# Optimization experiments

Measured on AMD Instinct MI355X. Metric: run time of the kernel, lower is better.

Reference implementation:

```python
import jax, jax.numpy as jnp
import numpy as np

B, C, W = 8, 128, 4096
REDUCTION = 8
D = C // REDUCTION  # 16


def setup_inputs() -> dict:
    key = jax.random.key(0)
    ks = jax.random.split(key, 7)
    scale = 0.05
    return {
        "x": jax.random.normal(ks[0], (B, C, W), dtype=jnp.float32),
        "Wq": jax.random.normal(ks[1], (D, C), dtype=jnp.float32) * scale,
        "bq": jax.random.normal(ks[2], (D,), dtype=jnp.float32) * scale,
        "Wk": jax.random.normal(ks[3], (D, C), dtype=jnp.float32) * scale,
        "bk": jax.random.normal(ks[4], (D,), dtype=jnp.float32) * scale,
        "Wv": jax.random.normal(ks[5], (C, C), dtype=jnp.float32) * scale,
        "bv": jax.random.normal(ks[6], (C,), dtype=jnp.float32) * scale,
    }


def reference(x, Wq, bq, Wk, bk, Wv, bv):
    # 1x1 Conv1d == per-position linear over channel axis
    q = jnp.einsum('dc,bcw->bdw', Wq, x) + bq[None, :, None]   # [B, D, W]
    k = jnp.einsum('dc,bcw->bdw', Wk, x) + bk[None, :, None]   # [B, D, W]
    v = jnp.einsum('oc,bcw->bow', Wv, x) + bv[None, :, None]   # [B, C, W]
    scale = D ** (-0.5)
    # scores[b,i,j] = q[b,:,i] . k[b,:,j]
    scores = jnp.einsum('bdi,bdj->bij', q, k) * scale          # [B, W, W]
    attn = jax.nn.softmax(scores, axis=-1)
    # torch.bmm(value, attn): context[b,c,w] = sum_j v[b,c,j] * attn[b,j,w]
    context = jnp.einsum('bcj,bjw->bcw', v, attn)              # [B, C, W]
    return context + x
```

## Files before the change

### kernel.cpp

```cpp
#include <hip/hip_runtime.h>

#define B_ 8
#define C_ 128
#define W_ 4096
#define D_ 16
#define SCALE2 0.3606737602222409f

typedef short bf16x8 __attribute__((ext_vector_type(8)));
typedef float f32x4 __attribute__((ext_vector_type(4)));

__device__ __forceinline__ unsigned short f2bf(float f) {
    unsigned int u = __float_as_uint(f);
    u += 0x7fffu + ((u >> 16) & 1u);
    return (unsigned short)(u >> 16);
}
__device__ __forceinline__ unsigned int pk2bf(float lo, float hi) {
    return __builtin_amdgcn_perm(__float_as_uint(hi), __float_as_uint(lo), 0x07060302u);
}
__device__ __forceinline__ bf16x8 u4_to_bf8(unsigned int a, unsigned int b,
                                            unsigned int c, unsigned int d) {
    union { uint4 u; bf16x8 v; } t;
    t.u = make_uint4(a, b, c, d);
    return t.v;
}
__device__ __forceinline__ bf16x8 exp2pack(f32x4 a, f32x4 b) {
    return u4_to_bf8(
        pk2bf(__builtin_amdgcn_exp2f(a[0]), __builtin_amdgcn_exp2f(a[1])),
        pk2bf(__builtin_amdgcn_exp2f(a[2]), __builtin_amdgcn_exp2f(a[3])),
        pk2bf(__builtin_amdgcn_exp2f(b[0]), __builtin_amdgcn_exp2f(b[1])),
        pk2bf(__builtin_amdgcn_exp2f(b[2]), __builtin_amdgcn_exp2f(b[3])));
}
__device__ __forceinline__ int xswz(int j, int c8) {
    return c8 ^ (j & 7) ^ ((j >> 3) & 7);
}

__global__ __launch_bounds__(256) void prep(
    const float* __restrict__ Wq, const float* __restrict__ Wk, const float* __restrict__ Wv,
    unsigned short* __restrict__ Wvbf, unsigned short* __restrict__ Wqkbf)
{
    int g = blockIdx.x * 256 + threadIdx.x;
    const float* src; unsigned short* dst; float sc = 1.0f;
    if (g < 4096)      { src = Wv + g * 4;            dst = Wvbf + g * 4; }
    else if (g < 4608) { int t = g - 4096; src = Wq + t * 4; dst = Wqkbf + t * 4; sc = SCALE2; }
    else               { int t = g - 4608; src = Wk + t * 4; dst = Wqkbf + 2048 + t * 4; }
    float4 v = *(const float4*)src;
    unsigned short h[4] = {f2bf(v.x * sc), f2bf(v.y * sc), f2bf(v.z * sc), f2bf(v.w * sc)};
    *(ushort4*)dst = *(ushort4*)h;
}

__global__ __launch_bounds__(256) void proj(
    const float* __restrict__ x, const unsigned short* __restrict__ Wvbf,
    const unsigned short* __restrict__ Wqkbf,
    const float* __restrict__ bqp, const float* __restrict__ bkp, const float* __restrict__ bvp,
    unsigned short* __restrict__ qws, unsigned short* __restrict__ kws,
    unsigned short* __restrict__ vws)
{
    __shared__ unsigned short xbf[64 * 128];
    __shared__ unsigned short outs[128 * 72];

    int b  = blockIdx.x & 7;
    int j0 = (blockIdx.x >> 3) * 64;
    int tid = threadIdx.x;
    int wid = tid >> 6, lane = tid & 63, n = lane & 15, q4 = lane >> 4;

#pragma unroll
    for (int i = 0; i < 8; i++) {
        int c = (tid >> 4) + 16 * i;
        int jc = (tid & 15) * 4;
        float4 t = *(const float4*)(x + (size_t)(b * C_ + c) * W_ + j0 + jc);
        float tv[4] = {t.x, t.y, t.z, t.w};
#pragma unroll
        for (int cc = 0; cc < 4; cc++) {
            int j = jc + cc;
            xbf[j * 128 + xswz(j, c >> 3) * 8 + (c & 7)] = f2bf(tv[cc]);
        }
    }
    __syncthreads();

    const f32x4 zero = {0.f, 0.f, 0.f, 0.f};
    f32x4 accv[2][4]; f32x4 accq = zero, acck = zero;
#pragma unroll
    for (int os = 0; os < 2; os++)
#pragma unroll
        for (int js = 0; js < 4; js++) accv[os][js] = zero;

#pragma unroll
    for (int kk = 0; kk < 128; kk += 32) {
        bf16x8 av[2], aqf, akf, bx[4];
#pragma unroll
        for (int os = 0; os < 2; os++)
            av[os] = *(const bf16x8*)(Wvbf + (wid * 32 + os * 16 + n) * 128 + kk + q4 * 8);
        aqf = *(const bf16x8*)(Wqkbf + n * 128 + kk + q4 * 8);
        akf = *(const bf16x8*)(Wqkbf + (16 + n) * 128 + kk + q4 * 8);
#pragma unroll
        for (int js = 0; js < 4; js++) {
            int j = js * 16 + n;
            bx[js] = *(const bf16x8*)&xbf[j * 128 + xswz(j, (kk >> 3) + q4) * 8];
        }
#pragma unroll
        for (int os = 0; os < 2; os++)
#pragma unroll
            for (int js = 0; js < 4; js++)
                accv[os][js] = __builtin_amdgcn_mfma_f32_16x16x32_bf16(av[os], bx[js], accv[os][js], 0, 0, 0);
        accq = __builtin_amdgcn_mfma_f32_16x16x32_bf16(aqf, bx[wid], accq, 0, 0, 0);
        acck = __builtin_amdgcn_mfma_f32_16x16x32_bf16(akf, bx[wid], acck, 0, 0, 0);
    }

    {
        int pos = j0 + wid * 16 + n;
        float q0 = accq[0] + bqp[q4 * 4 + 0] * SCALE2;
        float q1 = accq[1] + bqp[q4 * 4 + 1] * SCALE2;
        float q2 = accq[2] + bqp[q4 * 4 + 2] * SCALE2;
        float q3 = accq[3] + bqp[q4 * 4 + 3] * SCALE2;
        float k0 = acck[0] + bkp[q4 * 4 + 0];
        float k1 = acck[1] + bkp[q4 * 4 + 1];
        float k2 = acck[2] + bkp[q4 * 4 + 2];
        float k3 = acck[3] + bkp[q4 * 4 + 3];
        size_t base = ((size_t)(b * 4 + (q4 >> 1)) * W_ + pos) * 8 + (q4 & 1) * 4;
        *(uint2*)(qws + base) = make_uint2((unsigned)f2bf(q0) | ((unsigned)f2bf(q1) << 16),
                                           (unsigned)f2bf(q2) | ((unsigned)f2bf(q3) << 16));
        *(uint2*)(kws + base) = make_uint2((unsigned)f2bf(k0) | ((unsigned)f2bf(k1) << 16),
                                           (unsigned)f2bf(k2) | ((unsigned)f2bf(k3) << 16));
    }
    {
        int which = tid >> 7;
        int plane = 2 + ((tid >> 6) & 1);
        int pos = j0 + (tid & 63);
        unsigned short* basep = which ? kws : qws;
        uint4 z = make_uint4(0, 0, 0, 0);
        if (which == 1 && plane == 2) z.x = 0x3f80u;
        *(uint4*)(basep + ((size_t)(b * 4 + plane) * W_ + pos) * 8) = z;
    }

    float bvv[2][4];
#pragma unroll
    for (int os = 0; os < 2; os++)
#pragma unroll
        for (int r = 0; r < 4; r++) bvv[os][r] = bvp[wid * 32 + os * 16 + q4 * 4 + r];
#pragma unroll
    for (int os = 0; os < 2; os++)
#pragma unroll
        for (int js = 0; js < 4; js++)
#pragma unroll
            for (int r = 0; r < 4; r++) {
                int c = wid * 32 + os * 16 + q4 * 4 + r;
                int j = js * 16 + n;
                outs[c * 72 + j] = f2bf(accv[os][js][r] + bvv[os][r]);
            }
    __syncthreads();
    {
        int p = tid;
#pragma unroll
        for (int rep = 0; rep < 2; rep++, p += 256) {
            int jt_l = p >> 7;
            int c    = p & 127;
            const uint4* src = (const uint4*)&outs[c * 72 + jt_l * 16];
            unsigned short* dst = vws + ((size_t)((b * 256 + (j0 >> 4) + jt_l) * 128 + c)) * 16;
            *(uint4*)(dst + 0) = src[0];
            *(uint4*)(dst + 8) = src[1];
        }
    }
}

__global__ __launch_bounds__(256) void row_stats(
    const unsigned short* __restrict__ qws, const unsigned short* __restrict__ kws,
    float* __restrict__ rlp)
{
    int blk = blockIdx.x;
    int b = blk & 7;
    int j0 = ((blk >> 3) & 63) * 64;
    int wsp = blk >> 9;
    int t0 = wsp * 16;
    int tid = threadIdx.x;
    int wid = tid >> 6, lane = tid & 63, n = lane & 15, q4 = lane >> 4;

    const bf16x8* qbase = (const bf16x8*)qws + (size_t)(b * 4 + q4) * W_;
    const bf16x8* kbase = (const bf16x8*)kws + (size_t)(b * 4 + q4) * W_;
    bf16x8 aq = qbase[j0 + wid * 16 + n];
    const f32x4 zero = {0.f, 0.f, 0.f, 0.f};

    float lt[4] = {0.f, 0.f, 0.f, 0.f};
    bf16x8 k0[4], k1[4];
#pragma unroll
    for (int ws = 0; ws < 4; ws++) {
        k0[ws] = kbase[(t0 + 0) * 64 + ws * 16 + n];
        k1[ws] = kbase[(t0 + 1) * 64 + ws * 16 + n];
    }

#pragma unroll 2
    for (int t = 0; t < 8; t++) {
        f32x4 sa[4], sb[4];
#pragma unroll
        for (int ws = 0; ws < 4; ws++)
            sa[ws] = __builtin_amdgcn_mfma_f32_16x16x32_bf16(aq, k0[ws], zero, 0, 0, 0);
#pragma unroll
        for (int ws = 0; ws < 4; ws++)
            sb[ws] = __builtin_amdgcn_mfma_f32_16x16x32_bf16(aq, k1[ws], zero, 0, 0, 0);
        int ta = t0 + ((2 * t + 2) & 15), tb = t0 + ((2 * t + 3) & 15);
#pragma unroll
        for (int ws = 0; ws < 4; ws++) {
            k0[ws] = kbase[ta * 64 + ws * 16 + n];
            k1[ws] = kbase[tb * 64 + ws * 16 + n];
        }
#pragma unroll
        for (int ws = 0; ws < 4; ws++)
#pragma unroll
            for (int r = 0; r < 4; r++) {
                lt[r] += __builtin_amdgcn_exp2f(sa[ws][r]);
                lt[r] += __builtin_amdgcn_exp2f(sb[ws][r]);
            }
    }
#pragma unroll
    for (int mask = 1; mask < 16; mask <<= 1)
#pragma unroll
        for (int r = 0; r < 4; r++) lt[r] += __shfl_xor(lt[r], mask, 64);
    if (n == 0) {
        f32x4 l4 = {lt[0], lt[1], lt[2], lt[3]};
        *(f32x4*)(rlp + (size_t)wsp * 32768 + (size_t)b * W_ + j0 + wid * 16 + q4 * 4) = l4;
    }
}

__global__ __launch_bounds__(256) void finl(const float* __restrict__ rlp,
                                            unsigned short* __restrict__ qws)
{
    int g = blockIdx.x * 256 + threadIdx.x;
    int b = g >> 12, j = g & (W_ - 1);
    float l = rlp[g] + rlp[32768 + g] + rlp[65536 + g] + rlp[98304 + g];
    qws[((size_t)(b * 4 + 2) * W_ + j) * 8] = f2bf(-__builtin_amdgcn_logf(l));
}

__global__ __launch_bounds__(256, 2) void attn_out(
    const float* __restrict__ x, const unsigned short* __restrict__ qws,
    const unsigned short* __restrict__ kws, const unsigned short* __restrict__ vws,
    float* __restrict__ out)
{
    __shared__ float red[2][128 * 68];

    int b  = blockIdx.x & 7;
    int w0 = (blockIdx.x >> 3) * 64;
    int tid = threadIdx.x;
    int wid = tid >> 6, lane = tid & 63, n = lane & 15, q4 = lane >> 4;

    const bf16x8* qbase = (const bf16x8*)qws + (size_t)(b * 4 + q4) * W_;
    const bf16x8* kbase = (const bf16x8*)kws + (size_t)(b * 4 + q4) * W_;
    const unsigned short* vtb = vws + (size_t)b * 256 * 128 * 16;

    bf16x8 bk[4];
#pragma unroll
    for (int ws = 0; ws < 4; ws++) bk[ws] = kbase[w0 + ws * 16 + n];

    const f32x4 zero = {0.f, 0.f, 0.f, 0.f};
    f32x4 acc[8][4];
#pragma unroll
    for (int mt = 0; mt < 8; mt++)
#pragma unroll
        for (int nt = 0; nt < 4; nt++) acc[mt][nt] = zero;

    bf16x8 aqA = qbase[wid * 16 + n];
    bf16x8 aqB = qbase[64 + wid * 16 + n];
    uint2 vfA[8], vfB[8];
#pragma unroll
    for (int mt = 0; mt < 8; mt++) {
        int c = mt * 16 + n;
        vfA[mt] = *(const uint2*)(vtb + (size_t)((wid) * 128 + c) * 16 + q4 * 4);
        vfB[mt] = *(const uint2*)(vtb + (size_t)((wid + 4) * 128 + c) * 16 + q4 * 4);
    }
    f32x4 sA[4], sB[4];
#pragma unroll
    for (int ws = 0; ws < 4; ws++) {
        sA[ws] = __builtin_amdgcn_mfma_f32_16x16x32_bf16(aqA, bk[ws], zero, 0, 0, 0);
        sB[ws] = __builtin_amdgcn_mfma_f32_16x16x32_bf16(aqB, bk[ws], zero, 0, 0, 0);
    }
    aqA = qbase[128 + wid * 16 + n];
    aqB = qbase[128 + 64 + wid * 16 + n];
    bf16x8 bfrag[4];
#pragma unroll
    for (int ws = 0; ws < 4; ws++) bfrag[ws] = exp2pack(sA[ws], sB[ws]);

    for (int it = 0; it < 32; it++) {
        int itn = (it + 1) & 31;
        uint2 vfA_n[8], vfB_n[8];
        int jtA_n = itn * 8 + wid, jtB_n = jtA_n + 4;
#pragma unroll
        for (int mt = 0; mt < 8; mt++) {
            int c = mt * 16 + n;
            vfA_n[mt] = *(const uint2*)(vtb + (size_t)(jtA_n * 128 + c) * 16 + q4 * 4);
            vfB_n[mt] = *(const uint2*)(vtb + (size_t)(jtB_n * 128 + c) * 16 + q4 * 4);
        }
#pragma unroll
        for (int ws = 0; ws < 4; ws++) {
            sA[ws] = __builtin_amdgcn_mfma_f32_16x16x32_bf16(aqA, bk[ws], zero, 0, 0, 0);
            sB[ws] = __builtin_amdgcn_mfma_f32_16x16x32_bf16(aqB, bk[ws], zero, 0, 0, 0);
        }
        int itn2 = (it + 2) & 31;
        aqA = qbase[itn2 * 128 + wid * 16 + n];
        aqB = qbase[itn2 * 128 + 64 + wid * 16 + n];
#pragma unroll
        for (int mt = 0; mt < 8; mt++) {
            bf16x8 af = u4_to_bf8(vfA[mt].x, vfA[mt].y, vfB[mt].x, vfB[mt].y);
#pragma unroll
            for (int nt = 0; nt < 4; nt++)
                acc[mt][nt] = __builtin_amdgcn_mfma_f32_16x16x32_bf16(af, bfrag[nt], acc[mt][nt], 0, 0, 0);
        }
#pragma unroll
        for (int ws = 0; ws < 4; ws++) bfrag[ws] = exp2pack(sA[ws], sB[ws]);
#pragma unroll
        for (int mt = 0; mt < 8; mt++) { vfA[mt] = vfA_n[mt]; vfB[mt] = vfB_n[mt]; }
    }

    if (wid >= 2) {
        float* buf = red[wid - 2];
#pragma unroll
        for (int mt = 0; mt < 8; mt++)
#pragma unroll
            for (int nt = 0; nt < 4; nt++)
#pragma unroll
                for (int r = 0; r < 4; r++)
                    buf[(mt * 16 + q4 * 4 + r) * 68 + nt * 16 + n] = acc[mt][nt][r];
    }
    __syncthreads();
    if (wid < 2) {
        const float* buf = red[wid];
#pragma unroll
        for (int mt = 0; mt < 8; mt++)
#pragma unroll
            for (int nt = 0; nt < 4; nt++)
#pragma unroll
                for (int r = 0; r < 4; r++)
                    acc[mt][nt][r] += buf[(mt * 16 + q4 * 4 + r) * 68 + nt * 16 + n];
    }
    __syncthreads();
    if (wid == 1) {
        float* buf = red[0];
#pragma unroll
        for (int mt = 0; mt < 8; mt++)
#pragma unroll
            for (int nt = 0; nt < 4; nt++)
#pragma unroll
                for (int r = 0; r < 4; r++)
                    buf[(mt * 16 + q4 * 4 + r) * 68 + nt * 16 + n] = acc[mt][nt][r];
    }
    __syncthreads();
    if (wid == 0) {
        float* buf = red[0];
#pragma unroll
        for (int mt = 0; mt < 8; mt++)
#pragma unroll
            for (int nt = 0; nt < 4; nt++)
#pragma unroll
                for (int r = 0; r < 4; r++) {
                    int idx = (mt * 16 + q4 * 4 + r) * 68 + nt * 16 + n;
                    buf[idx] = acc[mt][nt][r] + buf[idx];
                }
    }
    __syncthreads();
    {
#pragma unroll
        for (int u = 0; u < 8; u++) {
            int k = tid + 256 * u;
            int c = k >> 4, wseg = (k & 15) * 4;
            size_t gidx = (size_t)(b * C_ + c) * W_ + w0 + wseg;
            float4 xv = *(const float4*)(x + gidx);
            const float* s = &red[0][c * 68 + wseg];
            float4 o = make_float4(s[0] + xv.x, s[1] + xv.y, s[2] + xv.z, s[3] + xv.w);
            *(float4*)(out + gidx) = o;
        }
    }
}

extern "C" void kernel_launch(void* const* d_in, const int* in_sizes, int n_in,
                              void* d_out, int out_size, void* d_ws, size_t ws_size,
                              hipStream_t stream)
{
    const float* x  = (const float*)d_in[0];
    const float* Wq = (const float*)d_in[1];
    const float* bq = (const float*)d_in[2];
    const float* Wk = (const float*)d_in[3];
    const float* bk = (const float*)d_in[4];
    const float* Wv = (const float*)d_in[5];
    const float* bv = (const float*)d_in[6];
    float* out = (float*)d_out;

    unsigned short* qws  = (unsigned short*)d_ws;
    unsigned short* kws  = qws + (size_t)1048576;
    unsigned short* vws  = kws + (size_t)1048576;
    unsigned short* Wvbf = vws + (size_t)4194304;
    unsigned short* Wqkbf = Wvbf + 16384;
    float* rlp = (float*)(Wqkbf + 4096);

    prep<<<20, 256, 0, stream>>>(Wq, Wk, Wv, Wvbf, Wqkbf);
    proj<<<512, 256, 0, stream>>>(x, Wvbf, Wqkbf, bq, bk, bv, qws, kws, vws);
    row_stats<<<2048, 256, 0, stream>>>(qws, kws, rlp);
    finl<<<128, 256, 0, stream>>>(rlp, qws);
    attn_out<<<512, 256, 0, stream>>>(x, qws, kws, vws, out);
}
```

Before: 167.3 us.

## Split proj into smaller position tiles and widen attn_out to 8 waves

The projection kernel now handles 32 positions per block instead of 64, launching twice as many blocks. Each wave computes either Q or K for one 16-position slice instead of both. The attention-output kernel moves from 4 to 8 waves per block, with each wave covering half as many key tiles, and uses a tree reduction over eight accumulators through two shared buffers. The goal is more parallelism and better latency hiding, at the cost of more reduction passes and barriers and lower per-CU block occupancy under launch bounds of 512,1.

```diff
diff --git a/kernel.cpp b/kernel.cpp
--- a/kernel.cpp
+++ b/kernel.cpp
@@ -55,18 +55,18 @@
     unsigned short* __restrict__ qws, unsigned short* __restrict__ kws,
     unsigned short* __restrict__ vws)
 {
-    __shared__ unsigned short xbf[64 * 128];
-    __shared__ unsigned short outs[128 * 72];
+    __shared__ unsigned short xbf[32 * 128];
+    __shared__ unsigned short outs[128 * 40];
 
     int b  = blockIdx.x & 7;
-    int j0 = (blockIdx.x >> 3) * 64;
+    int j0 = (blockIdx.x >> 3) * 32;
     int tid = threadIdx.x;
     int wid = tid >> 6, lane = tid & 63, n = lane & 15, q4 = lane >> 4;
 
 #pragma unroll
-    for (int i = 0; i < 8; i++) {
-        int c = (tid >> 4) + 16 * i;
-        int jc = (tid & 15) * 4;
+    for (int i = 0; i < 4; i++) {
+        int idx = tid + 256 * i;
+        int c = idx >> 3, jc = (idx & 7) * 4;
         float4 t = *(const float4*)(x + (size_t)(b * C_ + c) * W_ + j0 + jc);
         float tv[4] = {t.x, t.y, t.z, t.w};
 #pragma unroll
@@ -78,54 +78,52 @@
     __syncthreads();
 
     const f32x4 zero = {0.f, 0.f, 0.f, 0.f};
-    f32x4 accv[2][4]; f32x4 accq = zero, acck = zero;
+    f32x4 accv[2][2]; f32x4 accqk = zero;
 #pragma unroll
     for (int os = 0; os < 2; os++)
 #pragma unroll
-        for (int js = 0; js < 4; js++) accv[os][js] = zero;
+        for (int js = 0; js < 2; js++) accv[os][js] = zero;
+
+    int isK = wid >> 1;
+    int jsm = wid & 1;
 
 #pragma unroll
     for (int kk = 0; kk < 128; kk += 32) {
-        bf16x8 av[2], aqf, akf, bx[4];
+        bf16x8 av[2], aqkf, bx[2];
 #pragma unroll
         for (int os = 0; os < 2; os++)
             av[os] = *(const bf16x8*)(Wvbf + (wid * 32 + os * 16 + n) * 128 + kk + q4 * 8);
-        aqf = *(const bf16x8*)(Wqkbf + n * 128 + kk + q4 * 8);
-        akf = *(const bf16x8*)(Wqkbf + (16 + n) * 128 + kk + q4 * 8);
-#pragma unroll
-        for (int js = 0; js < 4; js++) {
+        aqkf = *(const bf16x8*)(Wqkbf + (isK * 16 + n) * 128 + kk + q4 * 8);
+#pragma unroll
+        for (int js = 0; js < 2; js++) {
             int j = js * 16 + n;
             bx[js] = *(const bf16x8*)&xbf[j * 128 + xswz(j, (kk >> 3) + q4) * 8];
         }
 #pragma unroll
         for (int os = 0; os < 2; os++)
 #pragma unroll
-            for (int js = 0; js < 4; js++)
+            for (int js = 0; js < 2; js++)
                 accv[os][js] = __builtin_amdgcn_mfma_f32_16x16x32_bf16(av[os], bx[js], accv[os][js], 0, 0, 0);
-        accq = __builtin_amdgcn_mfma_f32_16x16x32_bf16(aqf, bx[wid], accq, 0, 0, 0);
-        acck = __builtin_amdgcn_mfma_f32_16x16x32_bf16(akf, bx[wid], acck, 0, 0, 0);
+        accqk = __builtin_amdgcn_mfma_f32_16x16x32_bf16(aqkf, bx[jsm], accqk, 0, 0, 0);
     }
 
     {
-        int pos = j0 + wid * 16 + n;
-        float q0 = accq[0] + bqp[q4 * 4 + 0] * SCALE2;
-        float q1 = accq[1] + bqp[q4 * 4 + 1] * SCALE2;
-        float q2 = accq[2] + bqp[q4 * 4 + 2] * SCALE2;
-        float q3 = accq[3] + bqp[q4 * 4 + 3] * SCALE2;
-        float k0 = acck[0] + bkp[q4 * 4 + 0];
-        float k1 = acck[1] + bkp[q4 * 4 + 1];
-        float k2 = acck[2] + bkp[q4 * 4 + 2];
-        float k3 = acck[3] + bkp[q4 * 4 + 3];
+        int pos = j0 + jsm * 16 + n;
+        const float* bias = isK ? bkp : bqp;
+        float bsc = isK ? 1.0f : SCALE2;
+        float v0 = accqk[0] + bias[q4 * 4 + 0] * bsc;
+        float v1 = accqk[1] + bias[q4 * 4 + 1] * bsc;
+        float v2 = accqk[2] + bias[q4 * 4 + 2] * bsc;
+        float v3 = accqk[3] + bias[q4 * 4 + 3] * bsc;
+        unsigned short* basep = isK ? kws : qws;
         size_t base = ((size_t)(b * 4 + (q4 >> 1)) * W_ + pos) * 8 + (q4 & 1) * 4;
-        *(uint2*)(qws + base) = make_uint2((unsigned)f2bf(q0) | ((unsigned)f2bf(q1) << 16),
-                                           (unsigned)f2bf(q2) | ((unsigned)f2bf(q3) << 16));
-        *(uint2*)(kws + base) = make_uint2((unsigned)f2bf(k0) | ((unsigned)f2bf(k1) << 16),
-                                           (unsigned)f2bf(k2) | ((unsigned)f2bf(k3) << 16));
-    }
-    {
-        int which = tid >> 7;
-        int plane = 2 + ((tid >> 6) & 1);
-        int pos = j0 + (tid & 63);
+        *(uint2*)(basep + base) = make_uint2((unsigned)f2bf(v0) | ((unsigned)f2bf(v1) << 16),
+                                             (unsigned)f2bf(v2) | ((unsigned)f2bf(v3) << 16));
+    }
+    if (tid < 128) {
+        int which = tid >> 6;
+        int plane = 2 + ((tid >> 5) & 1);
+        int pos = j0 + (tid & 31);
         unsigned short* basep = which ? kws : qws;
         uint4 z = make_uint4(0, 0, 0, 0);
         if (which == 1 && plane == 2) z.x = 0x3f80u;
@@ -140,25 +138,21 @@
 #pragma unroll
     for (int os = 0; os < 2; os++)
 #pragma unroll
-        for (int js = 0; js < 4; js++)
+        for (int js = 0; js < 2; js++)
 #pragma unroll
             for (int r = 0; r < 4; r++) {
                 int c = wid * 32 + os * 16 + q4 * 4 + r;
                 int j = js * 16 + n;
-                outs[c * 72 + j] = f2bf(accv[os][js][r] + bvv[os][r]);
+                outs[c * 40 + j] = f2bf(accv[os][js][r] + bvv[os][r]);
             }
     __syncthreads();
     {
-        int p = tid;
-#pragma unroll
-        for (int rep = 0; rep < 2; rep++, p += 256) {
-            int jt_l = p >> 7;
-            int c    = p & 127;
-            const uint4* src = (const uint4*)&outs[c * 72 + jt_l * 16];
-            unsigned short* dst = vws + ((size_t)((b * 256 + (j0 >> 4) + jt_l) * 128 + c)) * 16;
-            *(uint4*)(dst + 0) = src[0];
-            *(uint4*)(dst + 8) = src[1];
-        }
+        int jt_l = tid >> 7;
+        int c    = tid & 127;
+        const uint4* src = (const uint4*)&outs[c * 40 + jt_l * 16];
+        unsigned short* dst = vws + ((size_t)((b * 256 + (j0 >> 4) + jt_l) * 128 + c)) * 16;
+        *(uint4*)(dst + 0) = src[0];
+        *(uint4*)(dst + 8) = src[1];
     }
 }
 
@@ -229,12 +223,13 @@
     qws[((size_t)(b * 4 + 2) * W_ + j) * 8] = f2bf(-__builtin_amdgcn_logf(l));
 }
 
-__global__ __launch_bounds__(256, 2) void attn_out(
+__global__ __launch_bounds__(512, 1) void attn_out(
     const float* __restrict__ x, const unsigned short* __restrict__ qws,
     const unsigned short* __restrict__ kws, const unsigned short* __restrict__ vws,
     float* __restrict__ out)
 {
-    __shared__ float red[2][128 * 68];
+    __shared__ float bufA[128 * 68];
+    __shared__ float bufB[128 * 68];
 
     int b  = blockIdx.x & 7;
     int w0 = (blockIdx.x >> 3) * 64;
@@ -256,14 +251,14 @@
 #pragma unroll
         for (int nt = 0; nt < 4; nt++) acc[mt][nt] = zero;
 
-    bf16x8 aqA = qbase[wid * 16 + n];
-    bf16x8 aqB = qbase[64 + wid * 16 + n];
+    bf16x8 aqA = qbase[wid * 32 + n];
+    bf16x8 aqB = qbase[wid * 32 + 16 + n];
     uint2 vfA[8], vfB[8];
 #pragma unroll
     for (int mt = 0; mt < 8; mt++) {
         int c = mt * 16 + n;
-        vfA[mt] = *(const uint2*)(vtb + (size_t)((wid) * 128 + c) * 16 + q4 * 4);
-        vfB[mt] = *(const uint2*)(vtb + (size_t)((wid + 4) * 128 + c) * 16 + q4 * 4);
+        vfA[mt] = *(const uint2*)(vtb + (size_t)((wid * 2 + 0) * 128 + c) * 16 + q4 * 4);
+        vfB[mt] = *(const uint2*)(vtb + (size_t)((wid * 2 + 1) * 128 + c) * 16 + q4 * 4);
     }
     f32x4 sA[4], sB[4];
 #pragma unroll
@@ -271,16 +266,16 @@
         sA[ws] = __builtin_amdgcn_mfma_f32_16x16x32_bf16(aqA, bk[ws], zero, 0, 0, 0);
         sB[ws] = __builtin_amdgcn_mfma_f32_16x16x32_bf16(aqB, bk[ws], zero, 0, 0, 0);
     }
-    aqA = qbase[128 + wid * 16 + n];
-    aqB = qbase[128 + 64 + wid * 16 + n];
+    aqA = qbase[256 + wid * 32 + n];
+    aqB = qbase[256 + wid * 32 + 16 + n];
     bf16x8 bfrag[4];
 #pragma unroll
     for (int ws = 0; ws < 4; ws++) bfrag[ws] = exp2pack(sA[ws], sB[ws]);
 
-    for (int it = 0; it < 32; it++) {
-        int itn = (it + 1) & 31;
+    for (int it = 0; it < 16; it++) {
+        int itn = (it + 1) & 15;
         uint2 vfA_n[8], vfB_n[8];
-        int jtA_n = itn * 8 + wid, jtB_n = jtA_n + 4;
+        int jtA_n = itn * 16 + wid * 2, jtB_n = jtA_n + 1;
 #pragma unroll
         for (int mt = 0; mt < 8; mt++) {
             int c = mt * 16 + n;
@@ -292,9 +287,9 @@
             sA[ws] = __builtin_amdgcn_mfma_f32_16x16x32_bf16(aqA, bk[ws], zero, 0, 0, 0);
             sB[ws] = __builtin_amdgcn_mfma_f32_16x16x32_bf16(aqB, bk[ws], zero, 0, 0, 0);
         }
-        int itn2 = (it + 2) & 31;
-        aqA = qbase[itn2 * 128 + wid * 16 + n];
-        aqB = qbase[itn2 * 128 + 64 + wid * 16 + n];
+        int itn2 = (it + 2) & 15;
+        aqA = qbase[itn2 * 256 + wid * 32 + n];
+        aqB = qbase[itn2 * 256 + wid * 32 + 16 + n];
 #pragma unroll
         for (int mt = 0; mt < 8; mt++) {
             bf16x8 af = u4_to_bf8(vfA[mt].x, vfA[mt].y, vfB[mt].x, vfB[mt].y);
@@ -308,63 +303,56 @@
         for (int mt = 0; mt < 8; mt++) { vfA[mt] = vfA_n[mt]; vfB[mt] = vfB_n[mt]; }
     }
 
-    if (wid >= 2) {
-        float* buf = red[wid - 2];
-#pragma unroll
-        for (int mt = 0; mt < 8; mt++)
-#pragma unroll
-            for (int nt = 0; nt < 4; nt++)
-#pragma unroll
-                for (int r = 0; r < 4; r++)
-                    buf[(mt * 16 + q4 * 4 + r) * 68 + nt * 16 + n] = acc[mt][nt][r];
-    }
-    __syncthreads();
-    if (wid < 2) {
-        const float* buf = red[wid];
-#pragma unroll
-        for (int mt = 0; mt < 8; mt++)
-#pragma unroll
-            for (int nt = 0; nt < 4; nt++)
-#pragma unroll
-                for (int r = 0; r < 4; r++)
-                    acc[mt][nt][r] += buf[(mt * 16 + q4 * 4 + r) * 68 + nt * 16 + n];
-    }
-    __syncthreads();
-    if (wid == 1) {
-        float* buf = red[0];
-#pragma unroll
-        for (int mt = 0; mt < 8; mt++)
-#pragma unroll
-            for (int nt = 0; nt < 4; nt++)
-#pragma unroll
-                for (int r = 0; r < 4; r++)
-                    buf[(mt * 16 + q4 * 4 + r) * 68 + nt * 16 + n] = acc[mt][nt][r];
-    }
-    __syncthreads();
-    if (wid == 0) {
-        float* buf = red[0];
-#pragma unroll
-        for (int mt = 0; mt < 8; mt++)
-#pragma unroll
-            for (int nt = 0; nt < 4; nt++)
-#pragma unroll
-                for (int r = 0; r < 4; r++) {
-                    int idx = (mt * 16 + q4 * 4 + r) * 68 + nt * 16 + n;
-                    buf[idx] = acc[mt][nt][r] + buf[idx];
-                }
-    }
-    __syncthreads();
-    {
-#pragma unroll
-        for (int u = 0; u < 8; u++) {
-            int k = tid + 256 * u;
-            int c = k >> 4, wseg = (k & 15) * 4;
-            size_t gidx = (size_t)(b * C_ + c) * W_ + w0 + wseg;
-            float4 xv = *(const float4*)(x + gidx);
-            const float* s = &red[0][c * 68 + wseg];
-            float4 o = make_float4(s[0] + xv.x, s[1] + xv.y, s[2] + xv.z, s[3] + xv.w);
-            *(float4*)(out + gidx) = o;
-        }
+#define WRITE_TILE(BUF)                                                          \
+    {                                                                            \
+        float* _b = (BUF);                                                       \
+        _Pragma("unroll") for (int mt = 0; mt < 8; mt++)                         \
+        _Pragma("unroll") for (int nt = 0; nt < 4; nt++)                         \
+        _Pragma("unroll") for (int r = 0; r < 4; r++)                            \
+            _b[(mt * 16 + q4 * 4 + r) * 68 + nt * 16 + n] = acc[mt][nt][r];      \
+    }
+#define ADD_TILE(BUF)                                                            \
+    {                                                                            \
+        const float* _b = (BUF);                                                 \
+        _Pragma("unroll") for (int mt = 0; mt < 8; mt++)                         \
+        _Pragma("unroll") for (int nt = 0; nt < 4; nt++)                         \
+        _Pragma("unroll") for (int r = 0; r < 4; r++)                            \
+            acc[mt][nt][r] += _b[(mt * 16 + q4 * 4 + r) * 68 + nt * 16 + n];     \
+    }
+    if (wid == 1) WRITE_TILE(bufA);
+    if (wid == 3) WRITE_TILE(bufB);
+    __syncthreads();
+    if (wid == 0) ADD_TILE(bufA);
+    if (wid == 2) ADD_TILE(bufB);
+    __syncthreads();
+    if (wid == 5) WRITE_TILE(bufA);
+    if (wid == 7) WRITE_TILE(bufB);
+    __syncthreads();
+    if (wid == 4) ADD_TILE(bufA);
+    if (wid == 6) ADD_TILE(bufB);
+    __syncthreads();
+    if (wid == 2) WRITE_TILE(bufA);
+    if (wid == 6) WRITE_TILE(bufB);
+    __syncthreads();
+    if (wid == 0) ADD_TILE(bufA);
+    if (wid == 4) ADD_TILE(bufB);
+    __syncthreads();
+    if (wid == 4) WRITE_TILE(bufA);
+    __syncthreads();
+    if (wid == 0) { ADD_TILE(bufA); WRITE_TILE(bufA); }
+    __syncthreads();
+#undef WRITE_TILE
+#undef ADD_TILE
+
+#pragma unroll
+    for (int u = 0; u < 4; u++) {
+        int k = tid + 512 * u;
+        int c = k >> 4, wseg = (k & 15) * 4;
+        size_t gidx = (size_t)(b * C_ + c) * W_ + w0 + wseg;
+        float4 xv = *(const float4*)(x + gidx);
+        const float* s = &bufA[c * 68 + wseg];
+        float4 o = make_float4(s[0] + xv.x, s[1] + xv.y, s[2] + xv.z, s[3] + xv.w);
+        *(float4*)(out + gidx) = o;
     }
 }
 
@@ -389,8 +377,8 @@
     float* rlp = (float*)(Wqkbf + 4096);
 
     prep<<<20, 256, 0, stream>>>(Wq, Wk, Wv, Wvbf, Wqkbf);
-    proj<<<512, 256, 0, stream>>>(x, Wvbf, Wqkbf, bq, bk, bv, qws, kws, vws);
+    proj<<<1024, 256, 0, stream>>>(x, Wvbf, Wqkbf, bq, bk, bv, qws, kws, vws);
     row_stats<<<2048, 256, 0, stream>>>(qws, kws, rlp);
     finl<<<128, 256, 0, stream>>>(rlp, qws);
-    attn_out<<<512, 256, 0, stream>>>(x, qws, kws, vws, out);
-}
+    attn_out<<<512, 512, 0, stream>>>(x, qws, kws, vws, out);
+}
```

New measurement: 171.8 us. 2.7% more time.

## Repack V workspace into contiguous 32-position fragments and halve proj tile

Applied to the files above, without the earlier changes.

The V workspace layout changes so each lane's A-fragment for the context MFMA (two 16-position halves) is a single contiguous 16-byte load instead of two 8-byte loads. The attn_out loop now loads next-iteration V fragments after the MFMAs with one uint4 per mt, dropping the register copy of a double buffer. In the projection kernel, positions per block shrink from 64 to 32 and the grid doubles, with Q/K work split across waves. The aims are fewer, wider global loads and lower register pressure in the hot loop; the cost is less latency hiding for V loads and more, smaller proj blocks.

```diff
diff --git a/kernel.cpp b/kernel.cpp
--- a/kernel.cpp
+++ b/kernel.cpp
@@ -21,6 +21,11 @@
                                             unsigned int c, unsigned int d) {
     union { uint4 u; bf16x8 v; } t;
     t.u = make_uint4(a, b, c, d);
+    return t.v;
+}
+__device__ __forceinline__ bf16x8 uint4_as_bf8(uint4 u) {
+    union { uint4 u; bf16x8 v; } t;
+    t.u = u;
     return t.v;
 }
 __device__ __forceinline__ bf16x8 exp2pack(f32x4 a, f32x4 b) {
@@ -55,18 +60,18 @@
     unsigned short* __restrict__ qws, unsigned short* __restrict__ kws,
     unsigned short* __restrict__ vws)
 {
-    __shared__ unsigned short xbf[64 * 128];
-    __shared__ unsigned short outs[128 * 72];
+    __shared__ unsigned short xbf[32 * 128];
+    __shared__ unsigned short outs[128 * 40];
 
     int b  = blockIdx.x & 7;
-    int j0 = (blockIdx.x >> 3) * 64;
+    int j0 = (blockIdx.x >> 3) * 32;
     int tid = threadIdx.x;
     int wid = tid >> 6, lane = tid & 63, n = lane & 15, q4 = lane >> 4;
 
 #pragma unroll
-    for (int i = 0; i < 8; i++) {
-        int c = (tid >> 4) + 16 * i;
-        int jc = (tid & 15) * 4;
+    for (int i = 0; i < 4; i++) {
+        int idx = tid + 256 * i;
+        int c = idx >> 3, jc = (idx & 7) * 4;
         float4 t = *(const float4*)(x + (size_t)(b * C_ + c) * W_ + j0 + jc);
         float tv[4] = {t.x, t.y, t.z, t.w};
 #pragma unroll
@@ -78,54 +83,52 @@
     __syncthreads();
 
     const f32x4 zero = {0.f, 0.f, 0.f, 0.f};
-    f32x4 accv[2][4]; f32x4 accq = zero, acck = zero;
+    f32x4 accv[2][2]; f32x4 accqk = zero;
 #pragma unroll
     for (int os = 0; os < 2; os++)
 #pragma unroll
-        for (int js = 0; js < 4; js++) accv[os][js] = zero;
+        for (int js = 0; js < 2; js++) accv[os][js] = zero;
+
+    int isK = wid >> 1;
+    int jsm = wid & 1;
 
 #pragma unroll
     for (int kk = 0; kk < 128; kk += 32) {
-        bf16x8 av[2], aqf, akf, bx[4];
+        bf16x8 av[2], aqkf, bx[2];
 #pragma unroll
         for (int os = 0; os < 2; os++)
             av[os] = *(const bf16x8*)(Wvbf + (wid * 32 + os * 16 + n) * 128 + kk + q4 * 8);
-        aqf = *(const bf16x8*)(Wqkbf + n * 128 + kk + q4 * 8);
-        akf = *(const bf16x8*)(Wqkbf + (16 + n) * 128 + kk + q4 * 8);
-#pragma unroll
-        for (int js = 0; js < 4; js++) {
+        aqkf = *(const bf16x8*)(Wqkbf + (isK * 16 + n) * 128 + kk + q4 * 8);
+#pragma unroll
+        for (int js = 0; js < 2; js++) {
             int j = js * 16 + n;
             bx[js] = *(const bf16x8*)&xbf[j * 128 + xswz(j, (kk >> 3) + q4) * 8];
         }
 #pragma unroll
         for (int os = 0; os < 2; os++)
 #pragma unroll
-            for (int js = 0; js < 4; js++)
+            for (int js = 0; js < 2; js++)
                 accv[os][js] = __builtin_amdgcn_mfma_f32_16x16x32_bf16(av[os], bx[js], accv[os][js], 0, 0, 0);
-        accq = __builtin_amdgcn_mfma_f32_16x16x32_bf16(aqf, bx[wid], accq, 0, 0, 0);
-        acck = __builtin_amdgcn_mfma_f32_16x16x32_bf16(akf, bx[wid], acck, 0, 0, 0);
+        accqk = __builtin_amdgcn_mfma_f32_16x16x32_bf16(aqkf, bx[jsm], accqk, 0, 0, 0);
     }
 
     {
-        int pos = j0 + wid * 16 + n;
-        float q0 = accq[0] + bqp[q4 * 4 + 0] * SCALE2;
-        float q1 = accq[1] + bqp[q4 * 4 + 1] * SCALE2;
-        float q2 = accq[2] + bqp[q4 * 4 + 2] * SCALE2;
-        float q3 = accq[3] + bqp[q4 * 4 + 3] * SCALE2;
-        float k0 = acck[0] + bkp[q4 * 4 + 0];
-        float k1 = acck[1] + bkp[q4 * 4 + 1];
-        float k2 = acck[2] + bkp[q4 * 4 + 2];
-        float k3 = acck[3] + bkp[q4 * 4 + 3];
+        int pos = j0 + jsm * 16 + n;
+        const float* bias = isK ? bkp : bqp;
+        float bsc = isK ? 1.0f : SCALE2;
+        float v0 = accqk[0] + bias[q4 * 4 + 0] * bsc;
+        float v1 = accqk[1] + bias[q4 * 4 + 1] * bsc;
+        float v2 = accqk[2] + bias[q4 * 4 + 2] * bsc;
+        float v3 = accqk[3] + bias[q4 * 4 + 3] * bsc;
+        unsigned short* basep = isK ? kws : qws;
         size_t base = ((size_t)(b * 4 + (q4 >> 1)) * W_ + pos) * 8 + (q4 & 1) * 4;
-        *(uint2*)(qws + base) = make_uint2((unsigned)f2bf(q0) | ((unsigned)f2bf(q1) << 16),
-                                           (unsigned)f2bf(q2) | ((unsigned)f2bf(q3) << 16));
-        *(uint2*)(kws + base) = make_uint2((unsigned)f2bf(k0) | ((unsigned)f2bf(k1) << 16),
-                                           (unsigned)f2bf(k2) | ((unsigned)f2bf(k3) << 16));
-    }
-    {
-        int which = tid >> 7;
-        int plane = 2 + ((tid >> 6) & 1);
-        int pos = j0 + (tid & 63);
+        *(uint2*)(basep + base) = make_uint2((unsigned)f2bf(v0) | ((unsigned)f2bf(v1) << 16),
+                                             (unsigned)f2bf(v2) | ((unsigned)f2bf(v3) << 16));
+    }
+    if (tid < 128) {
+        int which = tid >> 6;
+        int plane = 2 + ((tid >> 5) & 1);
+        int pos = j0 + (tid & 31);
         unsigned short* basep = which ? kws : qws;
         uint4 z = make_uint4(0, 0, 0, 0);
         if (which == 1 && plane == 2) z.x = 0x3f80u;
@@ -140,24 +143,24 @@
 #pragma unroll
     for (int os = 0; os < 2; os++)
 #pragma unroll
-        for (int js = 0; js < 4; js++)
+        for (int js = 0; js < 2; js++)
 #pragma unroll
             for (int r = 0; r < 4; r++) {
                 int c = wid * 32 + os * 16 + q4 * 4 + r;
                 int j = js * 16 + n;
-                outs[c * 72 + j] = f2bf(accv[os][js][r] + bvv[os][r]);
+                outs[c * 40 + j] = f2bf(accv[os][js][r] + bvv[os][r]);
             }
     __syncthreads();
     {
-        int p = tid;
-#pragma unroll
-        for (int rep = 0; rep < 2; rep++, p += 256) {
-            int jt_l = p >> 7;
-            int c    = p & 127;
-            const uint4* src = (const uint4*)&outs[c * 72 + jt_l * 16];
-            unsigned short* dst = vws + ((size_t)((b * 256 + (j0 >> 4) + jt_l) * 128 + c)) * 16;
-            *(uint4*)(dst + 0) = src[0];
-            *(uint4*)(dst + 8) = src[1];
+        int jp = j0 >> 5;
+#pragma unroll
+        for (int rep = 0; rep < 2; rep++) {
+            int idx = tid + 256 * rep;
+            int c = idx >> 2, q4g = idx & 3;
+            uint2 lo = *(const uint2*)&outs[c * 40 + q4g * 4];
+            uint2 hi = *(const uint2*)&outs[c * 40 + 16 + q4g * 4];
+            *(uint4*)(vws + ((((size_t)(b * 128 + jp) * 128 + c) * 4) + q4g) * 8) =
+                make_uint4(lo.x, lo.y, hi.x, hi.y);
         }
     }
 }
@@ -243,7 +246,7 @@
 
     const bf16x8* qbase = (const bf16x8*)qws + (size_t)(b * 4 + q4) * W_;
     const bf16x8* kbase = (const bf16x8*)kws + (size_t)(b * 4 + q4) * W_;
-    const unsigned short* vtb = vws + (size_t)b * 256 * 128 * 16;
+    const unsigned short* vtb = vws + (size_t)b * 128 * 128 * 32;
 
     bf16x8 bk[4];
 #pragma unroll
@@ -256,14 +259,13 @@
 #pragma unroll
         for (int nt = 0; nt < 4; nt++) acc[mt][nt] = zero;
 
-    bf16x8 aqA = qbase[wid * 16 + n];
-    bf16x8 aqB = qbase[64 + wid * 16 + n];
-    uint2 vfA[8], vfB[8];
+    bf16x8 aqA = qbase[wid * 32 + n];
+    bf16x8 aqB = qbase[wid * 32 + 16 + n];
+    uint4 vf[8];
 #pragma unroll
     for (int mt = 0; mt < 8; mt++) {
         int c = mt * 16 + n;
-        vfA[mt] = *(const uint2*)(vtb + (size_t)((wid) * 128 + c) * 16 + q4 * 4);
-        vfB[mt] = *(const uint2*)(vtb + (size_t)((wid + 4) * 128 + c) * 16 + q4 * 4);
+        vf[mt] = *(const uint4*)(vtb + (((size_t)(wid * 128 + c) * 4) + q4) * 8);
     }
     f32x4 sA[4], sB[4];
 #pragma unroll
@@ -271,41 +273,37 @@
         sA[ws] = __builtin_amdgcn_mfma_f32_16x16x32_bf16(aqA, bk[ws], zero, 0, 0, 0);
         sB[ws] = __builtin_amdgcn_mfma_f32_16x16x32_bf16(aqB, bk[ws], zero, 0, 0, 0);
     }
-    aqA = qbase[128 + wid * 16 + n];
-    aqB = qbase[128 + 64 + wid * 16 + n];
+    aqA = qbase[128 + wid * 32 + n];
+    aqB = qbase[128 + wid * 32 + 16 + n];
     bf16x8 bfrag[4];
 #pragma unroll
     for (int ws = 0; ws < 4; ws++) bfrag[ws] = exp2pack(sA[ws], sB[ws]);
 
     for (int it = 0; it < 32; it++) {
-        int itn = (it + 1) & 31;
-        uint2 vfA_n[8], vfB_n[8];
-        int jtA_n = itn * 8 + wid, jtB_n = jtA_n + 4;
-#pragma unroll
-        for (int mt = 0; mt < 8; mt++) {
-            int c = mt * 16 + n;
-            vfA_n[mt] = *(const uint2*)(vtb + (size_t)(jtA_n * 128 + c) * 16 + q4 * 4);
-            vfB_n[mt] = *(const uint2*)(vtb + (size_t)(jtB_n * 128 + c) * 16 + q4 * 4);
-        }
 #pragma unroll
         for (int ws = 0; ws < 4; ws++) {
             sA[ws] = __builtin_amdgcn_mfma_f32_16x16x32_bf16(aqA, bk[ws], zero, 0, 0, 0);
             sB[ws] = __builtin_amdgcn_mfma_f32_16x16x32_bf16(aqB, bk[ws], zero, 0, 0, 0);
         }
         int itn2 = (it + 2) & 31;
-        aqA = qbase[itn2 * 128 + wid * 16 + n];
-        aqB = qbase[itn2 * 128 + 64 + wid * 16 + n];
+        aqA = qbase[itn2 * 128 + wid * 32 + n];
+        aqB = qbase[itn2 * 128 + wid * 32 + 16 + n];
 #pragma unroll
         for (int mt = 0; mt < 8; mt++) {
-            bf16x8 af = u4_to_bf8(vfA[mt].x, vfA[mt].y, vfB[mt].x, vfB[mt].y);
+            bf16x8 af = uint4_as_bf8(vf[mt]);
 #pragma unroll
             for (int nt = 0; nt < 4; nt++)
                 acc[mt][nt] = __builtin_amdgcn_mfma_f32_16x16x32_bf16(af, bfrag[nt], acc[mt][nt], 0, 0, 0);
         }
+        int itn = (it + 1) & 31;
+        int jpn = itn * 4 + wid;
+#pragma unroll
+        for (int mt = 0; mt < 8; mt++) {
+            int c = mt * 16 + n;
+            vf[mt] = *(const uint4*)(vtb + (((size_t)(jpn * 128 + c) * 4) + q4) * 8);
+        }
 #pragma unroll
         for (int ws = 0; ws < 4; ws++) bfrag[ws] = exp2pack(sA[ws], sB[ws]);
-#pragma unroll
-        for (int mt = 0; mt < 8; mt++) { vfA[mt] = vfA_n[mt]; vfB[mt] = vfB_n[mt]; }
     }
 
     if (wid >= 2) {
@@ -389,7 +387,7 @@
     float* rlp = (float*)(Wqkbf + 4096);
 
     prep<<<20, 256, 0, stream>>>(Wq, Wk, Wv, Wvbf, Wqkbf);
-    proj<<<512, 256, 0, stream>>>(x, Wvbf, Wqkbf, bq, bk, bv, qws, kws, vws);
+    proj<<<1024, 256, 0, stream>>>(x, Wvbf, Wqkbf, bq, bk, bv, qws, kws, vws);
     row_stats<<<2048, 256, 0, stream>>>(qws, kws, rlp);
     finl<<<128, 256, 0, stream>>>(rlp, qws);
     attn_out<<<512, 256, 0, stream>>>(x, qws, kws, vws, out);
```

New measurement: 344.5 us. 2.06x slower.
